# Optimization experiments

Measured on AMD Instinct MI355X. Metric: run time of the kernel, lower is better.

The kernel has to match this reference:

```python
import jax, jax.numpy as jnp
import numpy as np

B, N, D, H, F = 2, 2048, 512, 8, 2048
HD = D // H
EPS = 1e-5

def _ln(x, g, b):
    m = jnp.mean(x, axis=-1, keepdims=True)
    v = jnp.mean((x - m) ** 2, axis=-1, keepdims=True)
    return (x - m) * jax.lax.rsqrt(v + EPS) * g + b

def setup_inputs() -> dict:
    key = jax.random.key(0)
    ks = jax.random.split(key, 20)
    def lin(k, din, dout, std=0.05):
        kw, kb = jax.random.split(k)
        return (jax.random.normal(kw, (din, dout), jnp.float32) * std,
                jnp.zeros((dout,), jnp.float32))
    Wq, bq = lin(ks[0], D, D)
    Wk, bk = lin(ks[1], D, D)
    Wv, bv = lin(ks[2], D, D)
    Wg, bg = lin(ks[3], D, D)
    Wo, bo = lin(ks[4], D, D)
    W1, b1 = lin(ks[5], D, F)
    W2, b2 = lin(ks[6], F, D)
    return {
        'x': jax.random.normal(ks[7], (B, N, D), jnp.float32),
        'attn_bias': jax.random.normal(ks[8], (B, N, N, H), jnp.float32) * 0.1,
        'attn_mask': jnp.zeros((B, N, N), jnp.bool_),
        'Wq': Wq, 'bq': bq, 'Wk': Wk, 'bk': bk, 'Wv': Wv, 'bv': bv,
        'Wg': Wg, 'bg': bg, 'Wo': Wo, 'bo': bo,
        'ln1_g': jnp.ones((D,), jnp.float32), 'ln1_b': jnp.zeros((D,), jnp.float32),
        'ln2_g': jnp.ones((D,), jnp.float32), 'ln2_b': jnp.zeros((D,), jnp.float32),
        'W1': W1, 'b1': b1, 'W2': W2, 'b2': b2,
    }

def reference(x, attn_bias, attn_mask, Wq, bq, Wk, bk, Wv, bv, Wg, bg, Wo, bo,
              ln1_g, ln1_b, ln2_g, ln2_b, W1, b1, W2, b2):
    scaling = HD ** -0.5
    # --- self-attention sublayer (pre-LN) ---
    y = _ln(x, ln1_g, ln1_b)
    q = (y @ Wq + bq).reshape(B, N, H, HD) * scaling
    k = (y @ Wk + bk).reshape(B, N, H, HD)
    v = (y @ Wv + bv).reshape(B, N, H, HD)
    u = y * jax.nn.sigmoid(y @ Wg + bg)            # GLU gating branch
    scores = jnp.einsum('bqhd,bkhd->bqkh', q, k)   # [B, Nq, Nk, H]
    scores = scores + attn_bias                    # attn_bias_type == 'add'
    scores = jnp.where(attn_mask[..., None], -jnp.inf, scores)
    w = jax.nn.softmax(scores, axis=2)             # softmax over keys
    attn = jnp.einsum('bqkh,bkhd->bqhd', w, v).reshape(B, N, D)
    attn = attn @ Wo + bo
    y = u + attn
    x = x + y                                      # residual (dropout = identity, eval)
    # --- FFN sublayer (pre-LN) ---
    y = _ln(x, ln2_g, ln2_b)
    y = jax.nn.gelu(y @ W1 + b1, approximate=False) @ W2 + b2
    return x + y
```

## Files before the change

### kernel.cpp

```cpp
#include <hip/hip_runtime.h>
#include <hip/hip_bf16.h>

#define DI __device__ __forceinline__

typedef __attribute__((ext_vector_type(8))) __bf16 bf16x8;
typedef __attribute__((ext_vector_type(4))) float f32x4;
typedef __attribute__((ext_vector_type(4))) unsigned short u16x4;
typedef __attribute__((ext_vector_type(8))) unsigned short u16x8;

DI unsigned short f2bs(float f) {
  __hip_bfloat16 h = __float2bfloat16(f);
  return __builtin_bit_cast(unsigned short, h);
}
DI float bs2f(unsigned short s) {
  return __bfloat162float(__builtin_bit_cast(__hip_bfloat16, s));
}
DI f32x4 mfma16(bf16x8 a, bf16x8 b, f32x4 c) {
  return __builtin_amdgcn_mfma_f32_16x16x32_bf16(a, b, c, 0, 0, 0);
}
DI void g2lds16(const void* g, void* l) {
  __builtin_amdgcn_global_load_lds(
      (__attribute__((address_space(1))) void*)(unsigned long long)g,
      (__attribute__((address_space(3))) void*)l, 16, 0, 0);
}

__global__ __launch_bounds__(256) void k_transw(const float* __restrict__ W,
                                                unsigned short* __restrict__ Wt,
                                                int K, int N) {
  __shared__ float tile[64][65];
  int tk = blockIdx.x * 64, tn = blockIdx.y * 64;
  int t = threadIdx.x;
#pragma unroll
  for (int i = 0; i < 16; ++i) {
    int idx = t + i * 256;
    int r = idx >> 6, c = idx & 63;
    tile[r][c] = W[(size_t)(tk + r) * N + tn + c];
  }
  __syncthreads();
#pragma unroll
  for (int i = 0; i < 16; ++i) {
    int idx = t + i * 256;
    int n = idx >> 6, kk = idx & 63;
    Wt[(size_t)(tn + n) * K + tk + kk] = f2bs(tile[kk][n]);
  }
}

__global__ __launch_bounds__(256) void k_bcat(const float* __restrict__ bq,
                                              const float* __restrict__ bk,
                                              const float* __restrict__ bv,
                                              const float* __restrict__ bg,
                                              float* __restrict__ bcat) {
  int t = blockIdx.x * 256 + threadIdx.x;
  const float* src = t < 512 ? bq : t < 1024 ? bk : t < 1536 ? bv : bg;
  bcat[t] = src[t & 511];
}

__global__ __launch_bounds__(256) void k_ln(const float* __restrict__ x,
                                            const float* __restrict__ g,
                                            const float* __restrict__ b,
                                            unsigned short* __restrict__ y) {
  int row = blockIdx.x, t = threadIdx.x;
  const float* xr = x + (size_t)row * 512;
  float a0 = xr[t], a1 = xr[t + 256];
  float s1 = a0 + a1, s2 = a0 * a0 + a1 * a1;
#pragma unroll
  for (int o = 32; o > 0; o >>= 1) {
    s1 += __shfl_down(s1, o);
    s2 += __shfl_down(s2, o);
  }
  __shared__ float r1[4], r2[4], bc[2];
  int w = t >> 6, l = t & 63;
  if (l == 0) { r1[w] = s1; r2[w] = s2; }
  __syncthreads();
  if (t == 0) {
    float t1 = r1[0] + r1[1] + r1[2] + r1[3];
    float t2 = r2[0] + r2[1] + r2[2] + r2[3];
    float m = t1 / 512.f;
    float v = t2 / 512.f - m * m;
    bc[0] = m;
    bc[1] = rsqrtf(v + 1e-5f);
  }
  __syncthreads();
  float m = bc[0], inv = bc[1];
  y[(size_t)row * 512 + t] = f2bs((a0 - m) * inv * g[t] + b[t]);
  y[(size_t)row * 512 + t + 256] = f2bs((a1 - m) * inv * g[t + 256] + b[t + 256]);
}

template <int BM>
__global__ __launch_bounds__(256) void k_gemm(
    const unsigned short* __restrict__ A, const unsigned short* __restrict__ Bt,
    const float* __restrict__ bias, int M, int N, int K, int mode,
    float* __restrict__ outf, unsigned short* __restrict__ outh,
    const float* __restrict__ add1, const float* __restrict__ add2,
    unsigned short* __restrict__ vtout) {
  constexpr int MI = BM / 32;
  __shared__ __align__(16) unsigned short lA[BM * 64];
  __shared__ __align__(16) unsigned short lB[64 * 64];
  int t = threadIdx.x, w = t >> 6, l = t & 63;
  int l15 = l & 15, lg = l >> 4;
  int m0 = blockIdx.x * BM, n0 = blockIdx.y * 64;
  int wm = (w >> 1) * (BM / 2), wn = (w & 1) * 32;
  f32x4 acc[MI][2] = {};
  int sr = l >> 3, scb = (l & 7) * 16;
  for (int k0 = 0; k0 < K; k0 += 64) {
#pragma unroll
    for (int c = 0; c < MI; ++c) {
      int row = w * (BM / 4) + sr + c * 8;
      g2lds16((const char*)A + ((size_t)(m0 + row) * K + k0) * 2 + scb,
              (char*)lA + w * (BM / 4) * 128 + c * 1024);
    }
#pragma unroll
    for (int c = 0; c < 2; ++c) {
      int row = w * 16 + sr + c * 8;
      g2lds16((const char*)Bt + ((size_t)(n0 + row) * K + k0) * 2 + scb,
              (char*)lB + w * 2048 + c * 1024);
    }
    __syncthreads();
#pragma unroll
    for (int kc = 0; kc < 2; ++kc) {
      bf16x8 af[MI], bfr[2];
#pragma unroll
      for (int i = 0; i < MI; ++i)
        af[i] = *(const bf16x8*)((const char*)lA + (wm + i * 16 + l15) * 128 + kc * 64 + lg * 16);
#pragma unroll
      for (int j = 0; j < 2; ++j)
        bfr[j] = *(const bf16x8*)((const char*)lB + (wn + j * 16 + l15) * 128 + kc * 64 + lg * 16);
#pragma unroll
      for (int i = 0; i < MI; ++i)
#pragma unroll
        for (int j = 0; j < 2; ++j)
          acc[i][j] = mfma16(af[i], bfr[j], acc[i][j]);
    }
    __syncthreads();
  }
#pragma unroll
  for (int i = 0; i < MI; ++i) {
#pragma unroll
    for (int j = 0; j < 2; ++j) {
      int col = n0 + wn + j * 16 + l15;
      int row0 = m0 + wm + i * 16 + lg * 4;
      float vals[4];
#pragma unroll
      for (int r = 0; r < 4; ++r) vals[r] = acc[i][j][r] + bias[col];
      if (mode == 6) {
        int sel = col >> 9, c5 = col & 511;
        if (sel == 2) {
          int hh = c5 >> 6, dd = c5 & 63, bb = row0 >> 11, nn = row0 & 2047;
          u16x4 pk;
#pragma unroll
          for (int r = 0; r < 4; ++r) pk[r] = f2bs(vals[r]);
          *(u16x4*)(vtout + (((size_t)(bb * 8 + hh) * 64 + dd) * 2048 + nn)) = pk;
        } else {
#pragma unroll
          for (int r = 0; r < 4; ++r) {
            size_t idx = (size_t)(row0 + r) * 512 + c5;
            if (sel == 0) outh[idx] = f2bs(vals[r] * 0.125f);
            else if (sel == 1) outh[2097152 + idx] = f2bs(vals[r]);
            else outf[idx] = bs2f(A[idx]) * (1.f / (1.f + __expf(-vals[r])));
          }
        }
      } else {
#pragma unroll
        for (int r = 0; r < 4; ++r) {
          size_t idx = (size_t)(row0 + r) * N + col;
          if (mode == 3) outf[idx] = vals[r] + add1[idx] + add2[idx];
          else if (mode == 4) outh[idx] = f2bs(0.5f * vals[r] * (1.f + erff(vals[r] * 0.70710678f)));
          else outf[idx] = vals[r] + add1[idx];
        }
      }
    }
  }
}

__global__ __launch_bounds__(512, 1) void k_attn7(
    const unsigned short* __restrict__ q, const unsigned short* __restrict__ kk,
    const unsigned short* __restrict__ vt, const float* __restrict__ bias,
    const unsigned char* __restrict__ mask, unsigned short* __restrict__ ao) {
  __shared__ __align__(16) char lsK[2][32768];
  __shared__ __align__(16) char lsV[2][32768];
  __shared__ __align__(16) char lsB[2][16 * 520];
  __shared__ __align__(16) unsigned short ls_p[8][16][36];

  int bid = blockIdx.x;
  int b = bid >> 7, qt = bid & 127;
  int q0 = qt * 16;
  int t = threadIdx.x, w = t >> 6, l = t & 63;
  int l15 = l & 15, lg = l >> 4;
  int h = w;

  bf16x8 qa0 = *(const bf16x8*)(q + ((size_t)(b * 2048 + q0 + l15) * 512 + h * 64 + lg * 8));
  bf16x8 qa1 = *(const bf16x8*)(q + ((size_t)(b * 2048 + q0 + l15) * 512 + h * 64 + 32 + lg * 8));

  union { bf16x8 v; unsigned short s[8]; } uo;
#pragma unroll
  for (int j = 0; j < 8; ++j) uo.s[j] = 0x3F80;
  const bf16x8 vones = uo.v;

  f32x4 oacc[4] = {};
  f32x4 lacc = {};

  const char* kptr[4];
  char* kdst[4];
#pragma unroll
  for (int i = 0; i < 4; ++i) {
    int fi = t + i * 512;
    int row = fi >> 6;
    int colb = ((fi & 63) * 16) ^ ((row & 7) << 4);
    kptr[i] = (const char*)kk + ((size_t)(b * 2048 + row) * 512) * 2 + colb;
    kdst[i] = (char*)0 + (i * 512 + w * 64) * 16;
  }
  const char* vptr[4];
#pragma unroll
  for (int i = 0; i < 4; ++i) {
    int fi = t + i * 512;
    int rv = fi >> 2;
    int dv = rv & 63, hv = rv >> 6;
    int slot = (fi & 3) ^ (dv & 3);
    vptr[i] = (const char*)vt + (((size_t)(b * 8 + hv) * 64 + dv) * 2048 + slot * 8) * 2;
  }
  int qq = t >> 5, kc = t & 31;
  const float* bptr = bias + ((size_t)(b * 2048 + q0 + qq) * 2048 + kc) * 8;
  const unsigned char* mptr = mask + (size_t)(b * 2048 + q0 + qq) * 2048 + kc;
  char* bdst = (char*)0 + qq * 520 + kc * 16;
  const unsigned short BN = f2bs(-1e30f);

#define STAGEKV(buf, kb)                                                     \
  do {                                                                       \
    _Pragma("unroll") for (int i = 0; i < 4; ++i)                            \
        g2lds16(kptr[i] + (size_t)(kb) * 1024, lsK[buf] + (size_t)kdst[i]);  \
    _Pragma("unroll") for (int i = 0; i < 4; ++i)                            \
        g2lds16(vptr[i] + (size_t)(kb) * 2, lsV[buf] + (size_t)kdst[i]);     \
  } while (0)
#define LOADB(BA, BB, MB, kb)                                                \
  do {                                                                       \
    BA = *(const float4*)(bptr + (size_t)(kb) * 8);                          \
    BB = *(const float4*)(bptr + (size_t)(kb) * 8 + 4);                      \
    MB = mptr[kb];                                                           \
  } while (0)
#define WRITEB(buf, BA, BB, MB)                                              \
  do {                                                                       \
    u16x8 o;                                                                 \
    if (MB) {                                                                \
      _Pragma("unroll") for (int j = 0; j < 8; ++j) o[j] = BN;               \
    } else {                                                                 \
      o[0] = f2bs(BA.x); o[1] = f2bs(BA.y); o[2] = f2bs(BA.z);               \
      o[3] = f2bs(BA.w); o[4] = f2bs(BB.x); o[5] = f2bs(BB.y);               \
      o[6] = f2bs(BB.z); o[7] = f2bs(BB.w);                                  \
    }                                                                        \
    *(u16x8*)(lsB[buf] + (size_t)bdst) = o;                                  \
  } while (0)
#define LDSK(buf, tt, kcc)                                                   \
  (*(const bf16x8*)(lsK[buf] + ((tt)*16 + l15) * 1024 +                      \
                    ((h * 128 + (kcc)*64 + lg * 16) ^ ((((tt)*16 + l15) & 7) << 4))))
#define LDSV(buf, dt)                                                        \
  (*(const bf16x8*)(lsV[buf] +                                               \
                    (((h * 64 + (dt)*16 + l15) * 4 +                         \
                      (lg ^ (((dt)*16 + l15) & 3))) * 16)))
#define COMPUTE(buf)                                                         \
  do {                                                                       \
    f32x4 sc0 = {}, sc1 = {};                                                \
    sc0 = mfma16(qa0, LDSK(buf, 0, 0), sc0);                                 \
    sc0 = mfma16(qa1, LDSK(buf, 0, 1), sc0);                                 \
    sc1 = mfma16(qa0, LDSK(buf, 1, 0), sc1);                                 \
    sc1 = mfma16(qa1, LDSK(buf, 1, 1), sc1);                                 \
    _Pragma("unroll") for (int r = 0; r < 4; ++r) {                          \
      int qr = lg * 4 + r;                                                   \
      float b0 = bs2f(*(const unsigned short*)(lsB[buf] + qr * 520 + l15 * 16 + h * 2));          \
      float b1 = bs2f(*(const unsigned short*)(lsB[buf] + qr * 520 + (l15 + 16) * 16 + h * 2));   \
      float p0 = __expf(sc0[r] + b0 - 8.0f);                                 \
      float p1 = __expf(sc1[r] + b1 - 8.0f);                                 \
      ls_p[w][qr][l15] = f2bs(p0);                                           \
      ls_p[w][qr][16 + l15] = f2bs(p1);                                      \
    }                                                                        \
    bf16x8 pa = *(const bf16x8*)&ls_p[w][l15][lg * 8];                       \
    oacc[0] = mfma16(pa, LDSV(buf, 0), oacc[0]);                             \
    oacc[1] = mfma16(pa, LDSV(buf, 1), oacc[1]);                             \
    oacc[2] = mfma16(pa, LDSV(buf, 2), oacc[2]);                             \
    oacc[3] = mfma16(pa, LDSV(buf, 3), oacc[3]);                             \
    lacc = mfma16(pa, vones, lacc);                                          \
  } while (0)

  float4 bA0, bA1, bB0, bB1;
  unsigned char mA, mB;
  LOADB(bA0, bA1, mA, 0);
  STAGEKV(0, 0);
  WRITEB(0, bA0, bA1, mA);
  __syncthreads();
  for (int it = 0; it < 64; it += 2) {
    int kb1 = (it + 1) * 32;
    LOADB(bB0, bB1, mB, kb1);
    STAGEKV(1, kb1);
    COMPUTE(0);
    WRITEB(1, bB0, bB1, mB);
    __syncthreads();
    int kb2 = (it + 2 < 64) ? (it + 2) * 32 : 0;
    LOADB(bA0, bA1, mA, kb2);
    STAGEKV(0, kb2);
    COMPUTE(1);
    WRITEB(0, bA0, bA1, mA);
    __syncthreads();
  }
#undef STAGEKV
#undef LOADB
#undef WRITEB
#undef LDSK
#undef LDSV
#undef COMPUTE

#pragma unroll
  for (int d = 0; d < 4; ++d)
#pragma unroll
    for (int r = 0; r < 4; ++r) {
      size_t row = (size_t)(b * 2048 + q0 + lg * 4 + r);
      ao[row * 512 + h * 64 + d * 16 + l15] = f2bs(oacc[d][r] / lacc[r]);
    }
}

extern "C" void kernel_launch(void* const* d_in, const int* in_sizes, int n_in,
                              void* d_out, int out_size, void* d_ws, size_t ws_size,
                              hipStream_t stream) {
  (void)in_sizes; (void)n_in; (void)out_size; (void)ws_size;
  const float* x = (const float*)d_in[0];
  const float* abias = (const float*)d_in[1];
  const unsigned char* amask = (const unsigned char*)d_in[2];
  const float* Wq = (const float*)d_in[3];
  const float* bq = (const float*)d_in[4];
  const float* Wk = (const float*)d_in[5];
  const float* bk = (const float*)d_in[6];
  const float* Wv = (const float*)d_in[7];
  const float* bv = (const float*)d_in[8];
  const float* Wg = (const float*)d_in[9];
  const float* bg = (const float*)d_in[10];
  const float* Wo = (const float*)d_in[11];
  const float* bo = (const float*)d_in[12];
  const float* ln1g = (const float*)d_in[13];
  const float* ln1b = (const float*)d_in[14];
  const float* ln2g = (const float*)d_in[15];
  const float* ln2b = (const float*)d_in[16];
  const float* W1 = (const float*)d_in[17];
  const float* b1 = (const float*)d_in[18];
  const float* W2 = (const float*)d_in[19];
  const float* b2 = (const float*)d_in[20];
  float* outp = (float*)d_out;

  char* ws = (char*)d_ws;
  const size_t MB = 1024 * 1024;

  unsigned short* qb = (unsigned short*)(ws + 0);
  unsigned short* kb = (unsigned short*)(ws + 4 * MB);
  unsigned short* ao = (unsigned short*)(ws + 8 * MB);
  unsigned short* y1 = (unsigned short*)(ws + 28 * MB);
  unsigned short* h1 = (unsigned short*)(ws + 0);
  float* u = (float*)(ws + 32 * MB);
  unsigned short* wcat = (unsigned short*)(ws + 40 * MB);
  unsigned short* wot = (unsigned short*)(ws + 42 * MB);
  unsigned short* w1t = (unsigned short*)(ws + 42 * MB + 512 * 1024);
  unsigned short* w2t = (unsigned short*)(ws + 44 * MB + 512 * 1024);
  float* bcat = (float*)(ws + 46 * MB + 512 * 1024);
  unsigned short* vtb = (unsigned short*)(ws + 48 * MB);
  float* x2 = (float*)d_out;

  k_transw<<<dim3(8, 8), 256, 0, stream>>>(Wq, wcat + 0 * 512 * 512, 512, 512);
  k_transw<<<dim3(8, 8), 256, 0, stream>>>(Wk, wcat + 1 * 512 * 512, 512, 512);
  k_transw<<<dim3(8, 8), 256, 0, stream>>>(Wv, wcat + 2 * 512 * 512, 512, 512);
  k_transw<<<dim3(8, 8), 256, 0, stream>>>(Wg, wcat + 3 * 512 * 512, 512, 512);
  k_transw<<<dim3(8, 8), 256, 0, stream>>>(Wo, wot, 512, 512);
  k_transw<<<dim3(8, 32), 256, 0, stream>>>(W1, w1t, 512, 2048);
  k_transw<<<dim3(32, 8), 256, 0, stream>>>(W2, w2t, 2048, 512);
  k_bcat<<<8, 256, 0, stream>>>(bq, bk, bv, bg, bcat);

  k_ln<<<4096, 256, 0, stream>>>(x, ln1g, ln1b, y1);
  k_gemm<128><<<dim3(32, 32), 256, 0, stream>>>(y1, wcat, bcat, 4096, 2048, 512, 6,
                                                u, qb, nullptr, nullptr, vtb);
  k_attn7<<<256, 512, 0, stream>>>(qb, kb, vtb, abias, amask, ao);
  k_gemm<64><<<dim3(64, 8), 256, 0, stream>>>(ao, wot, bo, 4096, 512, 512, 3,
                                              x2, nullptr, u, x, nullptr);
  k_ln<<<4096, 256, 0, stream>>>(x2, ln2g, ln2b, y1);
  k_gemm<128><<<dim3(32, 32), 256, 0, stream>>>(y1, w1t, b1, 4096, 2048, 512, 4,
                                                nullptr, h1, nullptr, nullptr, nullptr);
  k_gemm<64><<<dim3(64, 8), 256, 0, stream>>>(h1, w2t, b2, 4096, 512, 2048, 5,
                                              outp, nullptr, x2, nullptr, nullptr);
}
```

Before: 285.5 us.

## Load K/V fragments directly from global memory instead of LDS staging in attention

The attention kernel stops staging K and V tiles through double-buffered LDS with async global-to-LDS copies. Each wave now reads its own head's K and V MFMA fragments straight from global memory into registers, which drops 128KB of LDS. Only the bias tile stays in LDS, and it is synchronised with a lighter barrier that waits on lgkmcnt only. Block indexing is also interleaved across batches. The trade is uncoalesced global loads that sit exposed on the critical path, since they are issued inside the compute step with no prefetch, in exchange for less LDS traffic and cheaper synchronisation.

```diff
diff --git a/kernel.cpp b/kernel.cpp
--- a/kernel.cpp
+++ b/kernel.cpp
@@ -22,6 +22,12 @@
   __builtin_amdgcn_global_load_lds(
       (__attribute__((address_space(1))) void*)(unsigned long long)g,
       (__attribute__((address_space(3))) void*)l, 16, 0, 0);
+}
+DI void block_sync_lds() {
+  asm volatile("s_waitcnt lgkmcnt(0)" ::: "memory");
+  __builtin_amdgcn_sched_barrier(0);
+  __builtin_amdgcn_s_barrier();
+  __builtin_amdgcn_sched_barrier(0);
 }
 
 __global__ __launch_bounds__(256) void k_transw(const float* __restrict__ W,
@@ -172,17 +178,15 @@
   }
 }
 
-__global__ __launch_bounds__(512, 1) void k_attn7(
+__global__ __launch_bounds__(512, 1) void k_attn8(
     const unsigned short* __restrict__ q, const unsigned short* __restrict__ kk,
     const unsigned short* __restrict__ vt, const float* __restrict__ bias,
     const unsigned char* __restrict__ mask, unsigned short* __restrict__ ao) {
-  __shared__ __align__(16) char lsK[2][32768];
-  __shared__ __align__(16) char lsV[2][32768];
-  __shared__ __align__(16) char lsB[2][16 * 520];
+  __shared__ __align__(16) unsigned short lsB[2][16 * 260];
   __shared__ __align__(16) unsigned short ls_p[8][16][36];
 
   int bid = blockIdx.x;
-  int b = bid >> 7, qt = bid & 127;
+  int b = bid & 1, qt = bid >> 1;
   int q0 = qt * 16;
   int t = threadIdx.x, w = t >> 6, l = t & 63;
   int l15 = l & 15, lg = l >> 4;
@@ -199,38 +203,14 @@
   f32x4 oacc[4] = {};
   f32x4 lacc = {};
 
-  const char* kptr[4];
-  char* kdst[4];
-#pragma unroll
-  for (int i = 0; i < 4; ++i) {
-    int fi = t + i * 512;
-    int row = fi >> 6;
-    int colb = ((fi & 63) * 16) ^ ((row & 7) << 4);
-    kptr[i] = (const char*)kk + ((size_t)(b * 2048 + row) * 512) * 2 + colb;
-    kdst[i] = (char*)0 + (i * 512 + w * 64) * 16;
-  }
-  const char* vptr[4];
-#pragma unroll
-  for (int i = 0; i < 4; ++i) {
-    int fi = t + i * 512;
-    int rv = fi >> 2;
-    int dv = rv & 63, hv = rv >> 6;
-    int slot = (fi & 3) ^ (dv & 3);
-    vptr[i] = (const char*)vt + (((size_t)(b * 8 + hv) * 64 + dv) * 2048 + slot * 8) * 2;
-  }
+  const unsigned short* kbase = kk + ((size_t)(b * 2048) + l15) * 512 + h * 64 + lg * 8;
+  const unsigned short* vbase = vt + ((size_t)(b * 8 + h) * 64 + l15) * 2048 + lg * 8;
+
   int qq = t >> 5, kc = t & 31;
   const float* bptr = bias + ((size_t)(b * 2048 + q0 + qq) * 2048 + kc) * 8;
   const unsigned char* mptr = mask + (size_t)(b * 2048 + q0 + qq) * 2048 + kc;
-  char* bdst = (char*)0 + qq * 520 + kc * 16;
   const unsigned short BN = f2bs(-1e30f);
 
-#define STAGEKV(buf, kb)                                                     \
-  do {                                                                       \
-    _Pragma("unroll") for (int i = 0; i < 4; ++i)                            \
-        g2lds16(kptr[i] + (size_t)(kb) * 1024, lsK[buf] + (size_t)kdst[i]);  \
-    _Pragma("unroll") for (int i = 0; i < 4; ++i)                            \
-        g2lds16(vptr[i] + (size_t)(kb) * 2, lsV[buf] + (size_t)kdst[i]);     \
-  } while (0)
 #define LOADB(BA, BB, MB, kb)                                                \
   do {                                                                       \
     BA = *(const float4*)(bptr + (size_t)(kb) * 8);                          \
@@ -239,72 +219,72 @@
   } while (0)
 #define WRITEB(buf, BA, BB, MB)                                              \
   do {                                                                       \
-    u16x8 o;                                                                 \
+    u16x4 o0, o1;                                                            \
     if (MB) {                                                                \
-      _Pragma("unroll") for (int j = 0; j < 8; ++j) o[j] = BN;               \
+      o0[0] = o0[1] = o0[2] = o0[3] = BN;                                    \
+      o1[0] = o1[1] = o1[2] = o1[3] = BN;                                    \
     } else {                                                                 \
-      o[0] = f2bs(BA.x); o[1] = f2bs(BA.y); o[2] = f2bs(BA.z);               \
-      o[3] = f2bs(BA.w); o[4] = f2bs(BB.x); o[5] = f2bs(BB.y);               \
-      o[6] = f2bs(BB.z); o[7] = f2bs(BB.w);                                  \
+      o0[0] = f2bs(BA.x); o0[1] = f2bs(BA.y); o0[2] = f2bs(BA.z);            \
+      o0[3] = f2bs(BA.w); o1[0] = f2bs(BB.x); o1[1] = f2bs(BB.y);            \
+      o1[2] = f2bs(BB.z); o1[3] = f2bs(BB.w);                                \
     }                                                                        \
-    *(u16x8*)(lsB[buf] + (size_t)bdst) = o;                                  \
+    *(u16x4*)&lsB[buf][qq * 260 + kc * 8] = o0;                              \
+    *(u16x4*)&lsB[buf][qq * 260 + kc * 8 + 4] = o1;                          \
   } while (0)
-#define LDSK(buf, tt, kcc)                                                   \
-  (*(const bf16x8*)(lsK[buf] + ((tt)*16 + l15) * 1024 +                      \
-                    ((h * 128 + (kcc)*64 + lg * 16) ^ ((((tt)*16 + l15) & 7) << 4))))
-#define LDSV(buf, dt)                                                        \
-  (*(const bf16x8*)(lsV[buf] +                                               \
-                    (((h * 64 + (dt)*16 + l15) * 4 +                         \
-                      (lg ^ (((dt)*16 + l15) & 3))) * 16)))
-#define COMPUTE(buf)                                                         \
+#define COMPUTE(buf, kb)                                                     \
   do {                                                                       \
+    const unsigned short* kp = kbase + (size_t)(kb)*512;                     \
+    bf16x8 k00 = *(const bf16x8*)(kp);                                       \
+    bf16x8 k01 = *(const bf16x8*)(kp + 32);                                  \
+    bf16x8 k10 = *(const bf16x8*)(kp + 16 * 512);                            \
+    bf16x8 k11 = *(const bf16x8*)(kp + 16 * 512 + 32);                       \
+    const unsigned short* vp = vbase + (kb);                                 \
+    bf16x8 v0 = *(const bf16x8*)(vp);                                        \
+    bf16x8 v1 = *(const bf16x8*)(vp + 16 * 2048);                            \
+    bf16x8 v2 = *(const bf16x8*)(vp + 32 * 2048);                            \
+    bf16x8 v3 = *(const bf16x8*)(vp + 48 * 2048);                            \
     f32x4 sc0 = {}, sc1 = {};                                                \
-    sc0 = mfma16(qa0, LDSK(buf, 0, 0), sc0);                                 \
-    sc0 = mfma16(qa1, LDSK(buf, 0, 1), sc0);                                 \
-    sc1 = mfma16(qa0, LDSK(buf, 1, 0), sc1);                                 \
-    sc1 = mfma16(qa1, LDSK(buf, 1, 1), sc1);                                 \
+    sc0 = mfma16(qa0, k00, sc0);                                             \
+    sc0 = mfma16(qa1, k01, sc0);                                             \
+    sc1 = mfma16(qa0, k10, sc1);                                             \
+    sc1 = mfma16(qa1, k11, sc1);                                             \
     _Pragma("unroll") for (int r = 0; r < 4; ++r) {                          \
       int qr = lg * 4 + r;                                                   \
-      float b0 = bs2f(*(const unsigned short*)(lsB[buf] + qr * 520 + l15 * 16 + h * 2));          \
-      float b1 = bs2f(*(const unsigned short*)(lsB[buf] + qr * 520 + (l15 + 16) * 16 + h * 2));   \
+      float b0 = bs2f(lsB[buf][qr * 260 + l15 * 8 + h]);                     \
+      float b1 = bs2f(lsB[buf][qr * 260 + (l15 + 16) * 8 + h]);              \
       float p0 = __expf(sc0[r] + b0 - 8.0f);                                 \
       float p1 = __expf(sc1[r] + b1 - 8.0f);                                 \
       ls_p[w][qr][l15] = f2bs(p0);                                           \
       ls_p[w][qr][16 + l15] = f2bs(p1);                                      \
     }                                                                        \
     bf16x8 pa = *(const bf16x8*)&ls_p[w][l15][lg * 8];                       \
-    oacc[0] = mfma16(pa, LDSV(buf, 0), oacc[0]);                             \
-    oacc[1] = mfma16(pa, LDSV(buf, 1), oacc[1]);                             \
-    oacc[2] = mfma16(pa, LDSV(buf, 2), oacc[2]);                             \
-    oacc[3] = mfma16(pa, LDSV(buf, 3), oacc[3]);                             \
+    oacc[0] = mfma16(pa, v0, oacc[0]);                                       \
+    oacc[1] = mfma16(pa, v1, oacc[1]);                                       \
+    oacc[2] = mfma16(pa, v2, oacc[2]);                                       \
+    oacc[3] = mfma16(pa, v3, oacc[3]);                                       \
     lacc = mfma16(pa, vones, lacc);                                          \
   } while (0)
 
   float4 bA0, bA1, bB0, bB1;
   unsigned char mA, mB;
   LOADB(bA0, bA1, mA, 0);
-  STAGEKV(0, 0);
   WRITEB(0, bA0, bA1, mA);
-  __syncthreads();
+  LOADB(bB0, bB1, mB, 32);
+  block_sync_lds();
   for (int it = 0; it < 64; it += 2) {
-    int kb1 = (it + 1) * 32;
-    LOADB(bB0, bB1, mB, kb1);
-    STAGEKV(1, kb1);
-    COMPUTE(0);
-    WRITEB(1, bB0, bB1, mB);
-    __syncthreads();
     int kb2 = (it + 2 < 64) ? (it + 2) * 32 : 0;
     LOADB(bA0, bA1, mA, kb2);
-    STAGEKV(0, kb2);
-    COMPUTE(1);
+    COMPUTE(0, it * 32);
+    WRITEB(1, bB0, bB1, mB);
+    block_sync_lds();
+    int kb3 = (it + 3 < 64) ? (it + 3) * 32 : 0;
+    LOADB(bB0, bB1, mB, kb3);
+    COMPUTE(1, (it + 1) * 32);
     WRITEB(0, bA0, bA1, mA);
-    __syncthreads();
-  }
-#undef STAGEKV
+    block_sync_lds();
+  }
 #undef LOADB
 #undef WRITEB
-#undef LDSK
-#undef LDSV
 #undef COMPUTE
 
 #pragma unroll
@@ -372,7 +352,7 @@
   k_ln<<<4096, 256, 0, stream>>>(x, ln1g, ln1b, y1);
   k_gemm<128><<<dim3(32, 32), 256, 0, stream>>>(y1, wcat, bcat, 4096, 2048, 512, 6,
                                                 u, qb, nullptr, nullptr, vtb);
-  k_attn7<<<256, 512, 0, stream>>>(qb, kb, vtb, abias, amask, ao);
+  k_attn8<<<256, 512, 0, stream>>>(qb, kb, vtb, abias, amask, ao);
   k_gemm<64><<<dim3(64, 8), 256, 0, stream>>>(ao, wot, bo, 4096, 512, 512, 3,
                                               x2, nullptr, u, x, nullptr);
   k_ln<<<4096, 256, 0, stream>>>(x2, ln2g, ln2b, y1);
```

After: 289.9 us. About the same (+1.6%).

## Deepen attention bias prefetch and replace syncthreads with partial vmcnt waits

Applied to the files above, without the earlier changes.

The attention kernel now loads the bias/mask registers two K-blocks ahead instead of one, so global bias loads have a full compute iteration plus more to land. The __syncthreads calls are replaced by explicit s_waitcnt vmcnt(3) plus lgkmcnt(0) and a raw s_barrier, with sched_barrier fences. This lets the outstanding global loads for the next tiles stay in flight across the barrier instead of draining all vector memory ops. The risk is correctness depending on the exact count of outstanding loads (vmcnt(3) must match the issued load order), and the fences restrict compiler scheduling.

```diff
diff --git a/kernel.cpp b/kernel.cpp
--- a/kernel.cpp
+++ b/kernel.cpp
@@ -22,6 +22,18 @@
   __builtin_amdgcn_global_load_lds(
       (__attribute__((address_space(1))) void*)(unsigned long long)g,
       (__attribute__((address_space(3))) void*)l, 16, 0, 0);
+}
+#define SB __builtin_amdgcn_sched_barrier(0)
+DI void barrier_lgkm() {
+  asm volatile("s_waitcnt lgkmcnt(0)" ::: "memory");
+  SB;
+  __builtin_amdgcn_s_barrier();
+  SB;
+}
+DI void vm_guard3() {
+  SB;
+  asm volatile("s_waitcnt vmcnt(3)" ::: "memory");
+  SB;
 }
 
 __global__ __launch_bounds__(256) void k_transw(const float* __restrict__ W,
@@ -172,7 +184,7 @@
   }
 }
 
-__global__ __launch_bounds__(512, 1) void k_attn7(
+__global__ __launch_bounds__(512, 1) void k_attn14(
     const unsigned short* __restrict__ q, const unsigned short* __restrict__ kk,
     const unsigned short* __restrict__ vt, const float* __restrict__ bias,
     const unsigned char* __restrict__ mask, unsigned short* __restrict__ ao) {
@@ -280,25 +292,38 @@
     lacc = mfma16(pa, vones, lacc);                                          \
   } while (0)
 
-  float4 bA0, bA1, bB0, bB1;
+  float4 rA0, rA1, rB0, rB1;
   unsigned char mA, mB;
-  LOADB(bA0, bA1, mA, 0);
+  LOADB(rA0, rA1, mA, 0);
+  WRITEB(0, rA0, rA1, mA);
+  LOADB(rB0, rB1, mB, 32);
+  SB;
   STAGEKV(0, 0);
-  WRITEB(0, bA0, bA1, mA);
-  __syncthreads();
+  SB;
+  vm_guard3();
+  barrier_lgkm();
   for (int it = 0; it < 64; it += 2) {
     int kb1 = (it + 1) * 32;
-    LOADB(bB0, bB1, mB, kb1);
+    int kb2 = (it + 2 < 64) ? (it + 2) * 32 : 0;
+    int kb3 = (it + 3 < 64) ? (it + 3) * 32 : 0;
+    SB;
     STAGEKV(1, kb1);
+    SB;
+    LOADB(rA0, rA1, mA, kb2);
+    SB;
     COMPUTE(0);
-    WRITEB(1, bB0, bB1, mB);
-    __syncthreads();
-    int kb2 = (it + 2 < 64) ? (it + 2) * 32 : 0;
-    LOADB(bA0, bA1, mA, kb2);
+    WRITEB(1, rB0, rB1, mB);
+    vm_guard3();
+    barrier_lgkm();
+    SB;
     STAGEKV(0, kb2);
+    SB;
+    LOADB(rB0, rB1, mB, kb3);
+    SB;
     COMPUTE(1);
-    WRITEB(0, bA0, bA1, mA);
-    __syncthreads();
+    WRITEB(0, rA0, rA1, mA);
+    vm_guard3();
+    barrier_lgkm();
   }
 #undef STAGEKV
 #undef LOADB
@@ -372,7 +397,7 @@
   k_ln<<<4096, 256, 0, stream>>>(x, ln1g, ln1b, y1);
   k_gemm<128><<<dim3(32, 32), 256, 0, stream>>>(y1, wcat, bcat, 4096, 2048, 512, 6,
                                                 u, qb, nullptr, nullptr, vtb);
-  k_attn7<<<256, 512, 0, stream>>>(qb, kb, vtb, abias, amask, ao);
+  k_attn14<<<256, 512, 0, stream>>>(qb, kb, vtb, abias, amask, ao);
   k_gemm<64><<<dim3(64, 8), 256, 0, stream>>>(ao, wot, bo, 4096, 512, 512, 3,
                                               x2, nullptr, u, x, nullptr);
   k_ln<<<4096, 256, 0, stream>>>(x2, ln2g, ln2b, y1);
```

After: 269.0 us. -5.8%, faster.
